# Performance work log

Hardware: AMD Instinct MI355X
Metric: run time of the kernel (lower is better)

The kernel has to match this reference:

```python
import jax, jax.numpy as jnp
import numpy as np

EPS = 1e-6
K = 20
NUM_OBJECTS = 50
OBJ_FEAT = 256
C_DIM = 128
HIDDEN = 128


def vn_linear(x, W):
    # x: [B, C, 3, ...]; W: [O, C] -> [B, O, 3, ...]
    return jnp.einsum('oc,bc...->bo...', W, x)


def vn_leaky(x, Wdir, slope):
    d = vn_linear(x, Wdir)
    dot = jnp.sum(x * d, axis=2, keepdims=True)
    dsq = jnp.sum(d * d, axis=2, keepdims=True)
    x_neg = x - (dot / (dsq + EPS)) * d
    return slope * x + (1.0 - slope) * jnp.where(dot >= 0, x, x_neg)


def vn_linear_leaky(x, Wfeat, Wdir, slope):
    pf = vn_linear(x, Wfeat)
    d = vn_linear(x, Wdir)
    dot = jnp.sum(pf * d, axis=2, keepdims=True)
    dsq = jnp.sum(d * d, axis=2, keepdims=True)
    p_neg = pf - (dot / (dsq + EPS)) * d
    return slope * pf + (1.0 - slope) * jnp.where(dot >= 0, pf, p_neg)


def resblock(x, fc0, fc1, a0, a1, sc):
    net = vn_linear(vn_leaky(x, a0, 0.0), fc0)
    dx = vn_linear(vn_leaky(net, a1, 0.0), fc1)
    return vn_linear(x, sc) + dx


def get_graph_feature_cross(x, k):
    # x: [B, 3, N] -> edge features [B, 3, 3, N, k]
    inner = -2.0 * jnp.einsum('bdn,bdm->bnm', x, x)
    xx = jnp.sum(x * x, axis=1)                       # [B, N]
    neg_dist = -xx[:, :, None] - inner - xx[:, None, :]  # [B, N, N]
    idx = jax.lax.top_k(neg_dist, k)[1]               # [B, N, k] nearest neighbors
    xt = jnp.transpose(x, (0, 2, 1))                  # [B, N, 3]
    nbr = jax.vmap(lambda pts, ind: pts[ind])(xt, idx)  # [B, N, k, 3]
    ctr = jnp.broadcast_to(xt[:, :, None, :], nbr.shape)
    cross = jnp.cross(nbr, ctr)
    feat = jnp.stack([nbr - ctr, ctr, cross], axis=3)  # [B, N, k, 3, 3]
    return jnp.transpose(feat, (0, 3, 4, 1, 2))


def mlp2(zf, w0, w1, w2):
    h = jax.nn.relu(zf @ w0.T)
    h = jax.nn.relu(h @ w1.T)
    return h @ w2.T


def setup_inputs():
    key = jax.random.key(0)
    ks = jax.random.split(key, 24)
    B, N = 4, 4096

    def rn(k, shape):
        return jax.random.normal(k, shape, dtype=jnp.float32) * (1.0 / np.sqrt(shape[-1]))

    return {
        'p': jax.random.normal(ks[0], (B, N, 3), dtype=jnp.float32),
        'z_idxs': jax.random.randint(ks[1], (B,), 0, NUM_OBJECTS),
        'z': jax.random.normal(ks[2], (NUM_OBJECTS, OBJ_FEAT), dtype=jnp.float32),
        'hw0': rn(ks[3], (OBJ_FEAT, OBJ_FEAT)),
        'hw1': rn(ks[4], (OBJ_FEAT, OBJ_FEAT)),
        'hw2': rn(ks[5], (C_DIM * HIDDEN, OBJ_FEAT)),
        'hb0': rn(ks[6], (OBJ_FEAT, OBJ_FEAT)),
        'hb1': rn(ks[7], (OBJ_FEAT, OBJ_FEAT)),
        'hb2': rn(ks[8], (C_DIM, OBJ_FEAT)),
        'conv_pos_feat': rn(ks[9], (128, 3)),
        'conv_pos_dir': rn(ks[10], (128, 3)),
        'fc_pos_w': rn(ks[11], (2 * HIDDEN, 128)),
        'blk_fc0': rn(ks[12], (5, HIDDEN, 2 * HIDDEN)),
        'blk_fc1': rn(ks[13], (5, HIDDEN, HIDDEN)),
        'blk_act0': rn(ks[14], (5, 2 * HIDDEN, 2 * HIDDEN)),
        'blk_act1': rn(ks[15], (5, HIDDEN, HIDDEN)),
        'blk_sc': rn(ks[16], (5, HIDDEN, 2 * HIDDEN)),
        'actc_dir': rn(ks[17], (HIDDEN, HIDDEN)),
    }


def reference(p, z_idxs, z, hw0, hw1, hw2, hb0, hb1, hb2, conv_pos_feat,
              conv_pos_dir, fc_pos_w, blk_fc0, blk_fc1, blk_act0, blk_act1,
              blk_sc, actc_dir):
    B = p.shape[0]
    x = jnp.transpose(p, (0, 2, 1))                       # [B, 3, N]
    feat = get_graph_feature_cross(x, K)                  # [B, 3, 3, N, k]
    net = vn_linear_leaky(feat, conv_pos_feat, conv_pos_dir, 0.2)  # [B,128,3,N,k]
    net = jnp.mean(net, axis=-1)                          # [B,128,3,N]
    net = vn_linear(net, fc_pos_w)                        # [B,256,3,N]
    for i in range(5):
        net = resblock(net, blk_fc0[i], blk_fc1[i], blk_act0[i], blk_act1[i], blk_sc[i])
        if i < 4:
            pooled = jnp.mean(net, axis=-1, keepdims=True)
            net = jnp.concatenate([net, jnp.broadcast_to(pooled, net.shape)], axis=1)
    net = vn_leaky(jnp.mean(net, axis=-1), actc_dir, 0.2)  # [B, HIDDEN, 3]
    zf = z[z_idxs]                                        # [B, OBJ_FEAT]
    w = mlp2(zf, hw0, hw1, hw2).reshape(B, C_DIM, HIDDEN)  # hypernet weights
    b = mlp2(zf, hb0, hb1, hb2)                           # [B, C_DIM]
    c = jnp.einsum('bhd,bch->bcd', net, w) + b[:, :, None]  # [B, C_DIM, 3]
    return c
```

## Files before the change

kernel.cpp:

```cpp
#include <hip/hip_runtime.h>
#include <hip/hip_fp16.h>
#include <cstdint>
#include <cstddef>

#define NPTS 4096
#define BATCH 4
#define KNN 20

typedef __half f16;
using f32x4 = __attribute__((ext_vector_type(4))) float;
using f16x8 = __attribute__((ext_vector_type(8))) _Float16;

__global__ __launch_bounds__(256) void knn_kernel(const float* __restrict__ p,
                                                  int* __restrict__ idx_out) {
    __shared__ float pts[12288];
    const int tid  = threadIdx.x;
    const int wave = tid >> 6, lane = tid & 63;
    const int b  = blockIdx.x >> 10;
    const int nb = ((blockIdx.x & 1023) << 2) + wave;

    const float4* src4 = (const float4*)(p + (size_t)b * NPTS * 3);
    float4* dst4 = (float4*)pts;
    for (int i = tid; i < NPTS * 3 / 4; i += 256) dst4[i] = src4[i];
    __syncthreads();

    const float cx = pts[3 * nb], cy = pts[3 * nb + 1], cz = pts[3 * nb + 2];
    unsigned lst[4];
#pragma unroll
    for (int i = 0; i < 4; i++) lst[i] = 0xFFFFFFFFu;

    for (int t = 0; t < NPTS / 64; t++) {
        int m = (t << 6) + lane;
        float dx = pts[3 * m] - cx, dy = pts[3 * m + 1] - cy, dz = pts[3 * m + 2] - cz;
        float d = dx * dx + dy * dy + dz * dz;
        unsigned c = (__float_as_uint(d) & 0xFFFFF000u) | (unsigned)m;
#pragma unroll
        for (int j = 0; j < 4; j++) {
            unsigned lo = min(c, lst[j]);
            c = max(c, lst[j]);
            lst[j] = lo;
        }
    }

    unsigned lo = 0u, hi = 0xFFFFFFFFu;
    for (int it = 0; it < 32; it++) {
        unsigned mid = lo + ((hi - lo) >> 1);
        int cnt = __popcll(__ballot(lst[0] <= mid)) + __popcll(__ballot(lst[1] <= mid))
                + __popcll(__ballot(lst[2] <= mid)) + __popcll(__ballot(lst[3] <= mid));
        if (cnt >= KNN) hi = mid; else lo = mid + 1;
    }
    const unsigned T = hi;

    unsigned long long bl[4];
#pragma unroll
    for (int j = 0; j < 4; j++) bl[j] = __ballot(lst[j] <= T);
    const unsigned long long lmask = (lane == 63) ? ~0ull >> 1 : (1ull << lane) - 1;
    int base = 0;
    const size_t out_base = ((size_t)b * NPTS + nb) * KNN;
#pragma unroll
    for (int j = 0; j < 4; j++) {
        if (lst[j] <= T) {
            int pos = base + (int)__popcll(bl[j] & lmask);
            idx_out[out_base + pos] = (int)(lst[j] & 0xFFFu);
        }
        base += (int)__popcll(bl[j]);
    }
}

__global__ __launch_bounds__(128) void edgeconv_kernel(
    const float* __restrict__ p, const int* __restrict__ idx,
    const float* __restrict__ wf, const float* __restrict__ wd,
    f16* __restrict__ out) {
    __shared__ float e[KNN][9];
    const int col = blockIdx.x;
    const int b = col >> 12;
    const int tid = threadIdx.x;
    const float cx = p[(size_t)col * 3], cy = p[(size_t)col * 3 + 1], cz = p[(size_t)col * 3 + 2];
    if (tid < KNN) {
        int j = idx[(size_t)col * KNN + tid];
        const float* q = &p[((size_t)b * NPTS + j) * 3];
        float nx = q[0], ny = q[1], nz = q[2];
        e[tid][0] = nx - cx; e[tid][1] = ny - cy; e[tid][2] = nz - cz;
        e[tid][3] = cx;      e[tid][4] = cy;      e[tid][5] = cz;
        e[tid][6] = ny * cz - nz * cy;
        e[tid][7] = nz * cx - nx * cz;
        e[tid][8] = nx * cy - ny * cx;
    }
    __syncthreads();
    const int o = tid;
    const float f0 = wf[o * 3], f1 = wf[o * 3 + 1], f2 = wf[o * 3 + 2];
    const float g0 = wd[o * 3], g1 = wd[o * 3 + 1], g2 = wd[o * 3 + 2];
    float a0 = 0.f, a1 = 0.f, a2 = 0.f;
    for (int k = 0; k < KNN; k++) {
        float pf[3], dd[3];
#pragma unroll
        for (int s = 0; s < 3; s++) {
            pf[s] = f0 * e[k][s] + f1 * e[k][3 + s] + f2 * e[k][6 + s];
            dd[s] = g0 * e[k][s] + g1 * e[k][3 + s] + g2 * e[k][6 + s];
        }
        float dot = pf[0] * dd[0] + pf[1] * dd[1] + pf[2] * dd[2];
        float dsq = dd[0] * dd[0] + dd[1] * dd[1] + dd[2] * dd[2];
        float coef = dot * __builtin_amdgcn_rcpf(dsq + 1e-6f);
        bool pos = dot >= 0.f;
        float v0 = pos ? pf[0] : pf[0] - coef * dd[0];
        float v1 = pos ? pf[1] : pf[1] - coef * dd[1];
        float v2 = pos ? pf[2] : pf[2] - coef * dd[2];
        a0 += 0.2f * pf[0] + 0.8f * v0;
        a1 += 0.2f * pf[1] + 0.8f * v1;
        a2 += 0.2f * pf[2] + 0.8f * v2;
    }
    const float inv = 1.f / (float)KNN;
    out[((size_t)col * 3 + 0) * 128 + o] = __float2half(a0 * inv);
    out[((size_t)col * 3 + 1) * 128 + o] = __float2half(a1 * inv);
    out[((size_t)col * 3 + 2) * 128 + o] = __float2half(a2 * inv);
}

template <int KIN>
__global__ __launch_bounds__(256) void resblock_kernel(
    const uint16_t* __restrict__ INg,
    const uint16_t* __restrict__ Wfcp,
    const uint16_t* __restrict__ Wa0,
    const uint16_t* __restrict__ Wfc0,
    const uint16_t* __restrict__ Wa1,
    const uint16_t* __restrict__ Wsc,
    const uint16_t* __restrict__ Wfc1,
    const float* __restrict__ PBg,
    const float* __restrict__ BAg,
    const float* __restrict__ BSCg,
    f16* __restrict__ OUTg,
    float* __restrict__ PPg) {
    constexpr int XRB  = (KIN == 256) ? 528 : 272;
    constexpr int H0RB = 528;
    constexpr int MRB  = 272;
    constexpr int MBSZ = (KIN == 256) ? 48 * 272 : 0;
    constexpr int XSZ  = 48 * XRB;
    constexpr int CONSZ = (KIN == 128) ? 6144 : 0;
    constexpr int H0O  = MBSZ + XSZ + CONSZ;
    constexpr int MIDO = H0O + 48 * H0RB;
    __shared__ char lds[MIDO + 48 * MRB];
    char* MBs = lds;
    char* INs = lds + MBSZ;
    float* PBs  = (float*)(lds + MBSZ + XSZ);
    float* BAs  = PBs + 384;
    float* BSCs = BAs + 768;
    char* H0  = lds + H0O;
    char* MID = lds + MIDO;

    const int tid = threadIdx.x;
    const int lane = tid & 63;
    const int wc = tid >> 6;
    const int gr0 = blockIdx.x * 48;

    if (KIN == 128) {
        const int b = blockIdx.x >> 8;
        for (int i = tid; i < 384; i += 256) PBs[i]  = PBg[b * 384 + i];
        for (int i = tid; i < 768; i += 256) BAs[i]  = BAg[b * 768 + i];
        for (int i = tid; i < 384; i += 256) BSCs[i] = BSCg[b * 384 + i];
    }
    {
        char* dst = (KIN == 256) ? MBs : INs;
#pragma unroll
        for (int j = 0; j < 3; j++) {
            int chunk = tid + j * 256;
            int row = chunk >> 4, c16 = chunk & 15;
            f16x8 v = *(const f16x8*)(INg + (size_t)(gr0 + row) * 128 + c16 * 8);
            *(f16x8*)(dst + row * 272 + c16 * 16) = v;
        }
    }
    __syncthreads();

    if (KIN == 256) {
        f32x4 acc[3][4];
#pragma unroll
        for (int i = 0; i < 3; i++)
#pragma unroll
            for (int j = 0; j < 4; j++) acc[i][j] = (f32x4){0.f, 0.f, 0.f, 0.f};
#pragma unroll
        for (int ks = 0; ks < 4; ks++) {
            const int kb = ks * 64 + (lane >> 4) * 16;
            f16x8 af[3], bf[4];
#pragma unroll
            for (int mi = 0; mi < 3; mi++) {
                int r = mi * 16 + (lane & 15);
                af[mi] = *(const f16x8*)(MBs + r * 272 + kb);
            }
#pragma unroll
            for (int ni = 0; ni < 4; ni++) {
                int o = wc * 64 + ni * 16 + (lane & 15);
                bf[ni] = *(const f16x8*)(Wfcp + o * 128 + ks * 32 + (lane >> 4) * 8);
            }
#pragma unroll
            for (int mi = 0; mi < 3; mi++)
#pragma unroll
                for (int ni = 0; ni < 4; ni++)
                    acc[mi][ni] = __builtin_amdgcn_mfma_f32_16x16x32_f16(
                        af[mi], bf[ni], acc[mi][ni], 0, 0, 0);
        }
#pragma unroll
        for (int mi = 0; mi < 3; mi++)
#pragma unroll
            for (int ni = 0; ni < 4; ni++) {
                int col = wc * 64 + ni * 16 + (lane & 15);
#pragma unroll
                for (int r = 0; r < 4; r++) {
                    int row = mi * 16 + (lane >> 4) * 4 + r;
                    *(f16*)(INs + row * XRB + col * 2) = __float2half(acc[mi][ni][r]);
                }
            }
        __syncthreads();
    }

    {
        f32x4 acc[3][4];
#pragma unroll
        for (int i = 0; i < 3; i++)
#pragma unroll
            for (int j = 0; j < 4; j++) acc[i][j] = (f32x4){0.f, 0.f, 0.f, 0.f};
#pragma unroll
        for (int ks = 0; ks < KIN / 32; ks++) {
            const int kb = ks * 64 + (lane >> 4) * 16;
            f16x8 af[3], bf[4];
#pragma unroll
            for (int mi = 0; mi < 3; mi++) {
                int r = mi * 16 + (lane & 15);
                af[mi] = *(const f16x8*)(INs + r * XRB + kb);
            }
#pragma unroll
            for (int ni = 0; ni < 4; ni++) {
                int o = wc * 64 + ni * 16 + (lane & 15);
                bf[ni] = *(const f16x8*)(Wa0 + o * 256 + ks * 32 + (lane >> 4) * 8);
            }
#pragma unroll
            for (int mi = 0; mi < 3; mi++)
#pragma unroll
                for (int ni = 0; ni < 4; ni++)
                    acc[mi][ni] = __builtin_amdgcn_mfma_f32_16x16x32_f16(
                        af[mi], bf[ni], acc[mi][ni], 0, 0, 0);
        }
#pragma unroll
        for (int mi = 0; mi < 3; mi++)
#pragma unroll
            for (int ni = 0; ni < 4; ni++) {
                int col = wc * 64 + ni * 16 + (lane & 15);
#pragma unroll
                for (int r = 0; r < 4; r++) {
                    int row = mi * 16 + (lane >> 4) * 4 + r;
                    float v = acc[mi][ni][r];
                    if (KIN == 128) v += BAs[(row % 3) * 256 + col];
                    *(f16*)(H0 + row * H0RB + col * 2) = __float2half(v);
                }
            }
    }
    __syncthreads();
#pragma unroll
    for (int j = 0; j < 8; j++) {
        int it = tid + j * 256;
        int pnt = it >> 7, cp = it & 127;
        float xv[3][2], dv[3][2];
#pragma unroll
        for (int s = 0; s < 3; s++) {
            int row = pnt * 3 + s;
            __half2 d2 = *(const __half2*)(H0 + row * H0RB + cp * 4);
            dv[s][0] = __half2float(d2.x); dv[s][1] = __half2float(d2.y);
            if (KIN == 256) {
                __half2 x2 = *(const __half2*)(INs + row * XRB + cp * 4);
                xv[s][0] = __half2float(x2.x); xv[s][1] = __half2float(x2.y);
            } else {
                if (cp < 64) {
                    __half2 x2 = *(const __half2*)(INs + row * XRB + cp * 4);
                    xv[s][0] = __half2float(x2.x); xv[s][1] = __half2float(x2.y);
                } else {
                    xv[s][0] = PBs[s * 128 + (cp - 64) * 2];
                    xv[s][1] = PBs[s * 128 + (cp - 64) * 2 + 1];
                }
            }
        }
#pragma unroll
        for (int jj = 0; jj < 2; jj++) {
            float dot = xv[0][jj] * dv[0][jj] + xv[1][jj] * dv[1][jj] + xv[2][jj] * dv[2][jj];
            float dsq = dv[0][jj] * dv[0][jj] + dv[1][jj] * dv[1][jj] + dv[2][jj] * dv[2][jj];
            float coef = dot * __builtin_amdgcn_rcpf(dsq + 1e-6f);
            bool pos = dot >= 0.f;
#pragma unroll
            for (int s = 0; s < 3; s++)
                xv[s][jj] = pos ? xv[s][jj] : xv[s][jj] - coef * dv[s][jj];
        }
#pragma unroll
        for (int s = 0; s < 3; s++) {
            int row = pnt * 3 + s;
            __half2 h2;
            h2.x = __float2half(xv[s][0]);
            h2.y = __float2half(xv[s][1]);
            *(__half2*)(H0 + row * H0RB + cp * 4) = h2;
        }
    }
    __syncthreads();

    {
        f32x4 acc[3][2];
#pragma unroll
        for (int i = 0; i < 3; i++) { acc[i][0] = (f32x4){0,0,0,0}; acc[i][1] = (f32x4){0,0,0,0}; }
#pragma unroll
        for (int ks = 0; ks < 8; ks++) {
            const int kb = ks * 64 + (lane >> 4) * 16;
            f16x8 af[3], bf[2];
#pragma unroll
            for (int mi = 0; mi < 3; mi++) {
                int r = mi * 16 + (lane & 15);
                af[mi] = *(const f16x8*)(H0 + r * H0RB + kb);
            }
#pragma unroll
            for (int ni = 0; ni < 2; ni++) {
                int o = wc * 32 + ni * 16 + (lane & 15);
                bf[ni] = *(const f16x8*)(Wfc0 + o * 256 + ks * 32 + (lane >> 4) * 8);
            }
#pragma unroll
            for (int mi = 0; mi < 3; mi++)
#pragma unroll
                for (int ni = 0; ni < 2; ni++)
                    acc[mi][ni] = __builtin_amdgcn_mfma_f32_16x16x32_f16(
                        af[mi], bf[ni], acc[mi][ni], 0, 0, 0);
        }
#pragma unroll
        for (int mi = 0; mi < 3; mi++)
#pragma unroll
            for (int ni = 0; ni < 2; ni++) {
                int col = wc * 32 + ni * 16 + (lane & 15);
#pragma unroll
                for (int r = 0; r < 4; r++) {
                    int row = mi * 16 + (lane >> 4) * 4 + r;
                    *(f16*)(MID + row * MRB + col * 2) = __float2half(acc[mi][ni][r]);
                }
            }
    }
    __syncthreads();

    {
        f32x4 acc[3][2];
#pragma unroll
        for (int i = 0; i < 3; i++) { acc[i][0] = (f32x4){0,0,0,0}; acc[i][1] = (f32x4){0,0,0,0}; }
#pragma unroll
        for (int ks = 0; ks < 4; ks++) {
            const int kb = ks * 64 + (lane >> 4) * 16;
            f16x8 af[3], bf[2];
#pragma unroll
            for (int mi = 0; mi < 3; mi++) {
                int r = mi * 16 + (lane & 15);
                af[mi] = *(const f16x8*)(MID + r * MRB + kb);
            }
#pragma unroll
            for (int ni = 0; ni < 2; ni++) {
                int o = wc * 32 + ni * 16 + (lane & 15);
                bf[ni] = *(const f16x8*)(Wa1 + o * 128 + ks * 32 + (lane >> 4) * 8);
            }
#pragma unroll
            for (int mi = 0; mi < 3; mi++)
#pragma unroll
                for (int ni = 0; ni < 2; ni++)
                    acc[mi][ni] = __builtin_amdgcn_mfma_f32_16x16x32_f16(
                        af[mi], bf[ni], acc[mi][ni], 0, 0, 0);
        }
#pragma unroll
        for (int mi = 0; mi < 3; mi++)
#pragma unroll
            for (int ni = 0; ni < 2; ni++) {
                int col = wc * 32 + ni * 16 + (lane & 15);
#pragma unroll
                for (int r = 0; r < 4; r++) {
                    int row = mi * 16 + (lane >> 4) * 4 + r;
                    *(f16*)(H0 + row * MRB + col * 2) = __float2half(acc[mi][ni][r]);
                }
            }
    }
    __syncthreads();
#pragma unroll
    for (int j = 0; j < 4; j++) {
        int it = tid + j * 256;
        int pnt = it >> 6, cp = it & 63;
        float xv[3][2], dv[3][2];
#pragma unroll
        for (int s = 0; s < 3; s++) {
            int row = pnt * 3 + s;
            __half2 d2 = *(const __half2*)(H0 + row * MRB + cp * 4);
            __half2 x2 = *(const __half2*)(MID + row * MRB + cp * 4);
            dv[s][0] = __half2float(d2.x); dv[s][1] = __half2float(d2.y);
            xv[s][0] = __half2float(x2.x); xv[s][1] = __half2float(x2.y);
        }
#pragma unroll
        for (int jj = 0; jj < 2; jj++) {
            float dot = xv[0][jj] * dv[0][jj] + xv[1][jj] * dv[1][jj] + xv[2][jj] * dv[2][jj];
            float dsq = dv[0][jj] * dv[0][jj] + dv[1][jj] * dv[1][jj] + dv[2][jj] * dv[2][jj];
            float coef = dot * __builtin_amdgcn_rcpf(dsq + 1e-6f);
            bool pos = dot >= 0.f;
#pragma unroll
            for (int s = 0; s < 3; s++)
                xv[s][jj] = pos ? xv[s][jj] : xv[s][jj] - coef * dv[s][jj];
        }
#pragma unroll
        for (int s = 0; s < 3; s++) {
            int row = pnt * 3 + s;
            __half2 h2;
            h2.x = __float2half(xv[s][0]);
            h2.y = __float2half(xv[s][1]);
            *(__half2*)(H0 + row * MRB + cp * 4) = h2;
        }
    }
    __syncthreads();

    {
        f32x4 acc[3][2];
#pragma unroll
        for (int i = 0; i < 3; i++) { acc[i][0] = (f32x4){0,0,0,0}; acc[i][1] = (f32x4){0,0,0,0}; }
        constexpr int NKS = (KIN + 128) / 32;
#pragma unroll
        for (int ks = 0; ks < NKS; ks++) {
            const int kelem = ks * 32;
            f16x8 af[3], bf[2];
            if (kelem < KIN) {
                const int kb = kelem * 2 + (lane >> 4) * 16;
#pragma unroll
                for (int mi = 0; mi < 3; mi++) {
                    int r = mi * 16 + (lane & 15);
                    af[mi] = *(const f16x8*)(INs + r * XRB + kb);
                }
#pragma unroll
                for (int ni = 0; ni < 2; ni++) {
                    int o = wc * 32 + ni * 16 + (lane & 15);
                    bf[ni] = *(const f16x8*)(Wsc + o * 256 + kelem + (lane >> 4) * 8);
                }
            } else {
                const int kk = kelem - KIN;
                const int kb = kk * 2 + (lane >> 4) * 16;
#pragma unroll
                for (int mi = 0; mi < 3; mi++) {
                    int r = mi * 16 + (lane & 15);
                    af[mi] = *(const f16x8*)(H0 + r * MRB + kb);
                }
#pragma unroll
                for (int ni = 0; ni < 2; ni++) {
                    int o = wc * 32 + ni * 16 + (lane & 15);
                    bf[ni] = *(const f16x8*)(Wfc1 + o * 128 + kk + (lane >> 4) * 8);
                }
            }
#pragma unroll
            for (int mi = 0; mi < 3; mi++)
#pragma unroll
                for (int ni = 0; ni < 2; ni++)
                    acc[mi][ni] = __builtin_amdgcn_mfma_f32_16x16x32_f16(
                        af[mi], bf[ni], acc[mi][ni], 0, 0, 0);
        }
        float ps[2][3] = {};
#pragma unroll
        for (int mi = 0; mi < 3; mi++)
#pragma unroll
            for (int ni = 0; ni < 2; ni++) {
                int col = wc * 32 + ni * 16 + (lane & 15);
#pragma unroll
                for (int r = 0; r < 4; r++) {
                    int row = mi * 16 + (lane >> 4) * 4 + r;
                    float v = acc[mi][ni][r];
                    if (KIN == 128) v += BSCs[(row % 3) * 128 + col];
                    OUTg[(size_t)(gr0 + row) * 128 + col] = __float2half(v);
                    ps[ni][row % 3] += v;
                }
            }
#pragma unroll
        for (int ni = 0; ni < 2; ni++)
#pragma unroll
            for (int s = 0; s < 3; s++) {
                float x = ps[ni][s];
                x += __shfl_xor(x, 16, 64);
                x += __shfl_xor(x, 32, 64);
                ps[ni][s] = x;
            }
        if ((lane >> 4) == 0) {
#pragma unroll
            for (int ni = 0; ni < 2; ni++) {
                int col = wc * 32 + ni * 16 + (lane & 15);
#pragma unroll
                for (int s = 0; s < 3; s++)
                    PPg[(size_t)blockIdx.x * 384 + s * 128 + col] = ps[ni][s];
            }
        }
    }
}

__global__ __launch_bounds__(512) void poolbias_kernel(
    const float* __restrict__ PP, const f16* __restrict__ a0n, const f16* __restrict__ scn,
    float* __restrict__ PB, float* __restrict__ BA, float* __restrict__ BSC, int hasbias) {
    __shared__ float red[4][128];
    __shared__ float pl[128];
    const int bs = blockIdx.x;
    const int b = bs / 3, s = bs % 3;
    const int t = threadIdx.x;
    const int col = t & 127, seg = t >> 7;
    {
        float acc = 0.f;
        const float* base = PP + (size_t)(b * 256) * 384 + s * 128 + col;
        for (int k = seg * 64; k < seg * 64 + 64; k++) acc += base[(size_t)k * 384];
        red[seg][col] = acc;
    }
    __syncthreads();
    if (t < 128) {
        float a = (red[0][t] + red[1][t]) + (red[2][t] + red[3][t]);
        a *= (1.f / (float)NPTS);
        pl[t] = a;
        PB[bs * 128 + t] = a;
    }
    __syncthreads();
    if (!hasbias) return;
    if (t < 256) {
        float s2 = 0.f;
        for (int c = 0; c < 128; c++) s2 += __half2float(a0n[t * 256 + 128 + c]) * pl[c];
        BA[bs * 256 + t] = s2;
    } else if (t < 384) {
        int o = t - 256;
        float s2 = 0.f;
        for (int c = 0; c < 128; c++) s2 += __half2float(scn[o * 256 + 128 + c]) * pl[c];
        BSC[bs * 128 + o] = s2;
    }
}

__global__ void cvt_all(const float* __restrict__ fcpw, const float* __restrict__ act0,
                        const float* __restrict__ fc0, const float* __restrict__ act1,
                        const float* __restrict__ fc1, const float* __restrict__ scw,
                        f16* o_fcpw, f16* o_act0, f16* o_fc0, f16* o_act1, f16* o_fc1,
                        f16* o_scw) {
    int i = blockIdx.x * 256 + threadIdx.x;
    if (i < 32768) { o_fcpw[i] = __float2half(fcpw[i]); }
    else if (i < 360448) { int j = i - 32768;  o_act0[j] = __float2half(act0[j]); }
    else if (i < 524288) { int j = i - 360448; o_fc0[j]  = __float2half(fc0[j]); }
    else if (i < 606208) { int j = i - 524288; o_act1[j] = __float2half(act1[j]); }
    else if (i < 688128) { int j = i - 606208; o_fc1[j]  = __float2half(fc1[j]); }
    else                 { int j = i - 688128; o_scw[j]  = __float2half(scw[j]); }
}

__global__ __launch_bounds__(256) void hypermlp_kernel(
    const float* __restrict__ z, const int* __restrict__ zidx,
    const float* __restrict__ hw0, const float* __restrict__ hw1,
    const float* __restrict__ hb0, const float* __restrict__ hb1,
    const float* __restrict__ hb2,
    float* __restrict__ H2, float* __restrict__ BV) {
    __shared__ float zf[256], ta[256], tb[256];
    const int b = blockIdx.x, o = threadIdx.x;
    zf[o] = z[(size_t)zidx[b] * 256 + o];
    __syncthreads();
    float s = 0.f;
    for (int c = 0; c < 256; c++) s += zf[c] * hw0[o * 256 + c];
    ta[o] = fmaxf(s, 0.f);
    __syncthreads();
    s = 0.f;
    for (int c = 0; c < 256; c++) s += ta[c] * hw1[o * 256 + c];
    tb[o] = fmaxf(s, 0.f);
    __syncthreads();
    H2[(size_t)b * 256 + o] = tb[o];
    s = 0.f;
    for (int c = 0; c < 256; c++) s += zf[c] * hb0[o * 256 + c];
    __syncthreads();
    ta[o] = fmaxf(s, 0.f);
    __syncthreads();
    s = 0.f;
    for (int c = 0; c < 256; c++) s += ta[c] * hb1[o * 256 + c];
    __syncthreads();
    tb[o] = fmaxf(s, 0.f);
    __syncthreads();
    if (o < 128) {
        s = 0.f;
        for (int c = 0; c < 256; c++) s += tb[c] * hb2[o * 256 + c];
        BV[(size_t)b * 128 + o] = s;
    }
}

__global__ __launch_bounds__(256) void wmat_kernel(const float* __restrict__ H2,
                                                   const float* __restrict__ hw2,
                                                   float* __restrict__ WM) {
    __shared__ float h[256];
    const int b = blockIdx.y;
    const int row = blockIdx.x * 256 + threadIdx.x;
    h[threadIdx.x] = H2[(size_t)b * 256 + threadIdx.x];
    __syncthreads();
    float s = 0.f;
    for (int c = 0; c < 256; c++) s += h[c] * hw2[(size_t)row * 256 + c];
    WM[(size_t)b * 16384 + row] = s;
}

__global__ __launch_bounds__(384) void final_out_kernel(
    const float* __restrict__ pb, const float* __restrict__ actc,
    const float* __restrict__ WM, const float* __restrict__ BV,
    float* __restrict__ out) {
    __shared__ float pb2s[3][128];
    const int b = blockIdx.x;
    const int t = threadIdx.x;
    if (t < 128) {
        const int o = t;
        float d0 = 0.f, d1 = 0.f, d2 = 0.f;
        for (int c = 0; c < 128; c++) {
            float w = actc[o * 128 + c];
            d0 += w * pb[(size_t)(b * 3 + 0) * 128 + c];
            d1 += w * pb[(size_t)(b * 3 + 1) * 128 + c];
            d2 += w * pb[(size_t)(b * 3 + 2) * 128 + c];
        }
        float x0 = pb[(size_t)(b * 3 + 0) * 128 + o];
        float x1 = pb[(size_t)(b * 3 + 1) * 128 + o];
        float x2 = pb[(size_t)(b * 3 + 2) * 128 + o];
        float dot = x0 * d0 + x1 * d1 + x2 * d2;
        float dsq = d0 * d0 + d1 * d1 + d2 * d2;
        float coef = dot / (dsq + 1e-6f);
        bool pos = dot >= 0.f;
        float h0 = pos ? x0 : x0 - coef * d0;
        float h1 = pos ? x1 : x1 - coef * d1;
        float h2 = pos ? x2 : x2 - coef * d2;
        pb2s[0][o] = 0.2f * x0 + 0.8f * h0;
        pb2s[1][o] = 0.2f * x1 + 0.8f * h1;
        pb2s[2][o] = 0.2f * x2 + 0.8f * h2;
    }
    __syncthreads();
    const int cd = t / 3, d = t % 3;
    float s = BV[(size_t)b * 128 + cd];
    for (int h = 0; h < 128; h++)
        s += pb2s[d][h] * WM[(size_t)b * 16384 + cd * 128 + h];
    out[(size_t)b * 384 + cd * 3 + d] = s;
}

extern "C" void kernel_launch(void* const* d_in, const int* in_sizes, int n_in,
                              void* d_out, int out_size, void* d_ws, size_t ws_size,
                              hipStream_t stream) {
    (void)in_sizes; (void)n_in; (void)out_size; (void)ws_size;
    const float* p     = (const float*)d_in[0];
    const int*   zidx  = (const int*)d_in[1];
    const float* z     = (const float*)d_in[2];
    const float* hw0   = (const float*)d_in[3];
    const float* hw1   = (const float*)d_in[4];
    const float* hw2   = (const float*)d_in[5];
    const float* hb0   = (const float*)d_in[6];
    const float* hb1   = (const float*)d_in[7];
    const float* hb2   = (const float*)d_in[8];
    const float* cpf   = (const float*)d_in[9];
    const float* cpd   = (const float*)d_in[10];
    const float* fcpw  = (const float*)d_in[11];
    const float* fc0w  = (const float*)d_in[12];
    const float* fc1w  = (const float*)d_in[13];
    const float* act0  = (const float*)d_in[14];
    const float* act1  = (const float*)d_in[15];
    const float* scw   = (const float*)d_in[16];
    const float* actc  = (const float*)d_in[17];
    float* out = (float*)d_out;
    char* ws = (char*)d_ws;

    int*   IDX   = (int*)(ws + 0);
    f16*   MB    = (f16*)(ws + 1310720);
    f16*   MB2   = (f16*)(ws + 13893632);
    f16*   FCPW16= (f16*)(ws + 26476544);
    f16*   ACT0W = (f16*)(ws + 26542080);
    f16*   FC0W  = (f16*)(ws + 27197440);
    f16*   ACT1W = (f16*)(ws + 27525120);
    f16*   FC1W  = (f16*)(ws + 27688960);
    f16*   SCW16 = (f16*)(ws + 27852800);
    float* PP    = (float*)(ws + 28180480);
    float* PB    = (float*)(ws + 29753344);
    float* H2    = (float*)(ws + 29759488);
    float* BV    = (float*)(ws + 29763584);
    float* WM    = (float*)(ws + 29765632);
    float* BA    = (float*)(ws + 30027776);
    float* BSC   = (float*)(ws + 30040064);

    cvt_all<<<3328, 256, 0, stream>>>(fcpw, act0, fc0w, act1, fc1w, scw,
                                      FCPW16, ACT0W, FC0W, ACT1W, FC1W, SCW16);

    knn_kernel<<<BATCH * NPTS / 4, 256, 0, stream>>>(p, IDX);
    edgeconv_kernel<<<BATCH * NPTS, 128, 0, stream>>>(p, IDX, cpf, cpd, MB);

    resblock_kernel<256><<<1024, 256, 0, stream>>>(
        (const uint16_t*)MB, (const uint16_t*)FCPW16,
        (const uint16_t*)ACT0W, (const uint16_t*)FC0W,
        (const uint16_t*)ACT1W, (const uint16_t*)SCW16, (const uint16_t*)FC1W,
        nullptr, nullptr, nullptr, MB2, PP);
    poolbias_kernel<<<12, 512, 0, stream>>>(PP, ACT0W + 1 * 65536, SCW16 + 1 * 32768,
                                            PB, BA, BSC, 1);

    for (int i = 1; i < 5; i++) {
        const f16* a0h = ACT0W + (size_t)i * 256 * 256;
        const f16* sch = SCW16 + (size_t)i * 128 * 256;
        f16* in  = (i & 1) ? MB2 : MB;
        f16* ob  = (i & 1) ? MB : MB2;
        resblock_kernel<128><<<1024, 256, 0, stream>>>(
            (const uint16_t*)in, nullptr,
            (const uint16_t*)a0h,
            (const uint16_t*)(FC0W + (size_t)i * 128 * 256),
            (const uint16_t*)(ACT1W + (size_t)i * 128 * 128),
            (const uint16_t*)sch,
            (const uint16_t*)(FC1W + (size_t)i * 128 * 128),
            PB, BA, BSC, ob, PP);
        if (i < 4) {
            poolbias_kernel<<<12, 512, 0, stream>>>(
                PP, ACT0W + (size_t)(i + 1) * 65536, SCW16 + (size_t)(i + 1) * 32768,
                PB, BA, BSC, 1);
        } else {
            poolbias_kernel<<<12, 512, 0, stream>>>(PP, nullptr, nullptr, PB, BA, BSC, 0);
        }
    }

    hypermlp_kernel<<<4, 256, 0, stream>>>(z, zidx, hw0, hw1, hb0, hb1, hb2, H2, BV);
    wmat_kernel<<<dim3(64, 4), 256, 0, stream>>>(H2, hw2, WM);
    final_out_kernel<<<4, 384, 0, stream>>>(PB, actc, WM, BV, out);
}
```

Before: 409.8 us.

## Fuse shortcut GEMM into first resblock GEMM and simplify edgeconv math

The shortcut projection (Wsc) now accumulates in the same K-loop as the Wa0 GEMM, reusing the A fragments already loaded from LDS, so the final GEMM only covers the Wfc1 part. Bias tables BA and BSC are read straight from global memory instead of being staged in LDS, which shrinks shared memory. In the edgeconv kernel the constant center term is hoisted out of the k loop, the neighbour buffer shrinks to 6 floats, and the leaky-ReLU blend is rewritten with fewer operations. The trade-off is higher register pressure from keeping the shortcut accumulators live across the middle stage, which may cut occupancy.

After: 424.0 us. 3.5% more time.

```diff
diff --git a/kernel.cpp b/kernel.cpp
--- a/kernel.cpp
+++ b/kernel.cpp
@@ -71,7 +71,7 @@
     const float* __restrict__ p, const int* __restrict__ idx,
     const float* __restrict__ wf, const float* __restrict__ wd,
     f16* __restrict__ out) {
-    __shared__ float e[KNN][9];
+    __shared__ float e[KNN][6];
     const int col = blockIdx.x;
     const int b = col >> 12;
     const int tid = threadIdx.x;
@@ -81,33 +81,33 @@
         const float* q = &p[((size_t)b * NPTS + j) * 3];
         float nx = q[0], ny = q[1], nz = q[2];
         e[tid][0] = nx - cx; e[tid][1] = ny - cy; e[tid][2] = nz - cz;
-        e[tid][3] = cx;      e[tid][4] = cy;      e[tid][5] = cz;
-        e[tid][6] = ny * cz - nz * cy;
-        e[tid][7] = nz * cx - nx * cz;
-        e[tid][8] = nx * cy - ny * cx;
+        e[tid][3] = ny * cz - nz * cy;
+        e[tid][4] = nz * cx - nx * cz;
+        e[tid][5] = nx * cy - ny * cx;
     }
     __syncthreads();
     const int o = tid;
     const float f0 = wf[o * 3], f1 = wf[o * 3 + 1], f2 = wf[o * 3 + 2];
     const float g0 = wd[o * 3], g1 = wd[o * 3 + 1], g2 = wd[o * 3 + 2];
+    const float pc0 = f1 * cx, pc1 = f1 * cy, pc2 = f1 * cz;
+    const float gc0 = g1 * cx, gc1 = g1 * cy, gc2 = g1 * cz;
     float a0 = 0.f, a1 = 0.f, a2 = 0.f;
     for (int k = 0; k < KNN; k++) {
-        float pf[3], dd[3];
-#pragma unroll
-        for (int s = 0; s < 3; s++) {
-            pf[s] = f0 * e[k][s] + f1 * e[k][3 + s] + f2 * e[k][6 + s];
-            dd[s] = g0 * e[k][s] + g1 * e[k][3 + s] + g2 * e[k][6 + s];
-        }
-        float dot = pf[0] * dd[0] + pf[1] * dd[1] + pf[2] * dd[2];
-        float dsq = dd[0] * dd[0] + dd[1] * dd[1] + dd[2] * dd[2];
-        float coef = dot * __builtin_amdgcn_rcpf(dsq + 1e-6f);
-        bool pos = dot >= 0.f;
-        float v0 = pos ? pf[0] : pf[0] - coef * dd[0];
-        float v1 = pos ? pf[1] : pf[1] - coef * dd[1];
-        float v2 = pos ? pf[2] : pf[2] - coef * dd[2];
-        a0 += 0.2f * pf[0] + 0.8f * v0;
-        a1 += 0.2f * pf[1] + 0.8f * v1;
-        a2 += 0.2f * pf[2] + 0.8f * v2;
+        float d0 = e[k][0], d1 = e[k][1], d2 = e[k][2];
+        float c0 = e[k][3], c1 = e[k][4], c2 = e[k][5];
+        float pf0 = fmaf(f0, d0, fmaf(f2, c0, pc0));
+        float pf1 = fmaf(f0, d1, fmaf(f2, c1, pc1));
+        float pf2 = fmaf(f0, d2, fmaf(f2, c2, pc2));
+        float dd0 = fmaf(g0, d0, fmaf(g2, c0, gc0));
+        float dd1 = fmaf(g0, d1, fmaf(g2, c1, gc1));
+        float dd2 = fmaf(g0, d2, fmaf(g2, c2, gc2));
+        float dot = pf0 * dd0 + pf1 * dd1 + pf2 * dd2;
+        float dsq = dd0 * dd0 + dd1 * dd1 + dd2 * dd2;
+        float w = 0.8f * dot * __builtin_amdgcn_rcpf(dsq + 1e-6f);
+        w = (dot >= 0.f) ? 0.f : w;
+        a0 += pf0 - w * dd0;
+        a1 += pf1 - w * dd1;
+        a2 += pf2 - w * dd2;
     }
     const float inv = 1.f / (float)KNN;
     out[((size_t)col * 3 + 0) * 128 + o] = __float2half(a0 * inv);
@@ -134,15 +134,13 @@
     constexpr int MRB  = 272;
     constexpr int MBSZ = (KIN == 256) ? 48 * 272 : 0;
     constexpr int XSZ  = 48 * XRB;
-    constexpr int CONSZ = (KIN == 128) ? 6144 : 0;
-    constexpr int H0O  = MBSZ + XSZ + CONSZ;
+    constexpr int PBSZ = (KIN == 128) ? 1536 : 0;
+    constexpr int H0O  = MBSZ + XSZ + PBSZ;
     constexpr int MIDO = H0O + 48 * H0RB;
     __shared__ char lds[MIDO + 48 * MRB];
     char* MBs = lds;
     char* INs = lds + MBSZ;
-    float* PBs  = (float*)(lds + MBSZ + XSZ);
-    float* BAs  = PBs + 384;
-    float* BSCs = BAs + 768;
+    float* PBs = (float*)(lds + MBSZ + XSZ);
     char* H0  = lds + H0O;
     char* MID = lds + MIDO;
 
@@ -150,12 +148,10 @@
     const int lane = tid & 63;
     const int wc = tid >> 6;
     const int gr0 = blockIdx.x * 48;
+    const int b = blockIdx.x >> 8;
 
     if (KIN == 128) {
-        const int b = blockIdx.x >> 8;
-        for (int i = tid; i < 384; i += 256) PBs[i]  = PBg[b * 384 + i];
-        for (int i = tid; i < 768; i += 256) BAs[i]  = BAg[b * 768 + i];
-        for (int i = tid; i < 384; i += 256) BSCs[i] = BSCg[b * 384 + i];
+        for (int i = tid; i < 384; i += 256) PBs[i] = PBg[b * 384 + i];
     }
     {
         char* dst = (KIN == 256) ? MBs : INs;
@@ -210,6 +206,9 @@
         __syncthreads();
     }
 
+    f32x4 accS[3][2];
+#pragma unroll
+    for (int i = 0; i < 3; i++) { accS[i][0] = (f32x4){0,0,0,0}; accS[i][1] = (f32x4){0,0,0,0}; }
     {
         f32x4 acc[3][4];
 #pragma unroll
@@ -219,7 +218,7 @@
 #pragma unroll
         for (int ks = 0; ks < KIN / 32; ks++) {
             const int kb = ks * 64 + (lane >> 4) * 16;
-            f16x8 af[3], bf[4];
+            f16x8 af[3], bf[4], bs[2];
 #pragma unroll
             for (int mi = 0; mi < 3; mi++) {
                 int r = mi * 16 + (lane & 15);
@@ -231,11 +230,21 @@
                 bf[ni] = *(const f16x8*)(Wa0 + o * 256 + ks * 32 + (lane >> 4) * 8);
             }
 #pragma unroll
-            for (int mi = 0; mi < 3; mi++)
+            for (int ni = 0; ni < 2; ni++) {
+                int o = wc * 32 + ni * 16 + (lane & 15);
+                bs[ni] = *(const f16x8*)(Wsc + o * 256 + ks * 32 + (lane >> 4) * 8);
+            }
+#pragma unroll
+            for (int mi = 0; mi < 3; mi++) {
 #pragma unroll
                 for (int ni = 0; ni < 4; ni++)
                     acc[mi][ni] = __builtin_amdgcn_mfma_f32_16x16x32_f16(
                         af[mi], bf[ni], acc[mi][ni], 0, 0, 0);
+#pragma unroll
+                for (int ni = 0; ni < 2; ni++)
+                    accS[mi][ni] = __builtin_amdgcn_mfma_f32_16x16x32_f16(
+                        af[mi], bs[ni], accS[mi][ni], 0, 0, 0);
+            }
         }
 #pragma unroll
         for (int mi = 0; mi < 3; mi++)
@@ -246,7 +255,7 @@
                 for (int r = 0; r < 4; r++) {
                     int row = mi * 16 + (lane >> 4) * 4 + r;
                     float v = acc[mi][ni][r];
-                    if (KIN == 128) v += BAs[(row % 3) * 256 + col];
+                    if (KIN == 128) v += BAg[b * 768 + (row % 3) * 256 + col];
                     *(f16*)(H0 + row * H0RB + col * 2) = __float2half(v);
                 }
             }
@@ -408,46 +417,26 @@
     __syncthreads();
 
     {
-        f32x4 acc[3][2];
-#pragma unroll
-        for (int i = 0; i < 3; i++) { acc[i][0] = (f32x4){0,0,0,0}; acc[i][1] = (f32x4){0,0,0,0}; }
-        constexpr int NKS = (KIN + 128) / 32;
-#pragma unroll
-        for (int ks = 0; ks < NKS; ks++) {
-            const int kelem = ks * 32;
+#pragma unroll
+        for (int ks = 0; ks < 4; ks++) {
+            const int kb = ks * 64 + (lane >> 4) * 16;
             f16x8 af[3], bf[2];
-            if (kelem < KIN) {
-                const int kb = kelem * 2 + (lane >> 4) * 16;
-#pragma unroll
-                for (int mi = 0; mi < 3; mi++) {
-                    int r = mi * 16 + (lane & 15);
-                    af[mi] = *(const f16x8*)(INs + r * XRB + kb);
-                }
-#pragma unroll
-                for (int ni = 0; ni < 2; ni++) {
-                    int o = wc * 32 + ni * 16 + (lane & 15);
-                    bf[ni] = *(const f16x8*)(Wsc + o * 256 + kelem + (lane >> 4) * 8);
-                }
-            } else {
-                const int kk = kelem - KIN;
-                const int kb = kk * 2 + (lane >> 4) * 16;
-#pragma unroll
-                for (int mi = 0; mi < 3; mi++) {
-                    int r = mi * 16 + (lane & 15);
-                    af[mi] = *(const f16x8*)(H0 + r * MRB + kb);
-                }
-#pragma unroll
-                for (int ni = 0; ni < 2; ni++) {
-                    int o = wc * 32 + ni * 16 + (lane & 15);
-                    bf[ni] = *(const f16x8*)(Wfc1 + o * 128 + kk + (lane >> 4) * 8);
-                }
+#pragma unroll
+            for (int mi = 0; mi < 3; mi++) {
+                int r = mi * 16 + (lane & 15);
+                af[mi] = *(const f16x8*)(H0 + r * MRB + kb);
+            }
+#pragma unroll
+            for (int ni = 0; ni < 2; ni++) {
+                int o = wc * 32 + ni * 16 + (lane & 15);
+                bf[ni] = *(const f16x8*)(Wfc1 + o * 128 + ks * 32 + (lane >> 4) * 8);
             }
 #pragma unroll
             for (int mi = 0; mi < 3; mi++)
 #pragma unroll
                 for (int ni = 0; ni < 2; ni++)
-                    acc[mi][ni] = __builtin_amdgcn_mfma_f32_16x16x32_f16(
-                        af[mi], bf[ni], acc[mi][ni], 0, 0, 0);
+                    accS[mi][ni] = __builtin_amdgcn_mfma_f32_16x16x32_f16(
+                        af[mi], bf[ni], accS[mi][ni], 0, 0, 0);
         }
         float ps[2][3] = {};
 #pragma unroll
@@ -458,8 +447,8 @@
 #pragma unroll
                 for (int r = 0; r < 4; r++) {
                     int row = mi * 16 + (lane >> 4) * 4 + r;
-                    float v = acc[mi][ni][r];
-                    if (KIN == 128) v += BSCs[(row % 3) * 128 + col];
+                    float v = accS[mi][ni][r];
+                    if (KIN == 128) v += BSCg[b * 384 + (row % 3) * 128 + col];
                     OUTg[(size_t)(gr0 + row) * 128 + col] = __float2half(v);
                     ps[ni][row % 3] += v;
                 }
```
